# Performance work log

Measured on AMD Instinct MI355X. Metric: run time of the kernel, lower is better.

Reference implementation:

```python
import jax, jax.numpy as jnp
import numpy as np

N, E = 32768, 1048576          # nodes, edges (avg degree 32)
IN, H, OUT = 128, 128, 40       # in_channels, hidden_channels, out_channels
L, R = 3, 16                    # num_layers, n_rules
EPS = 1e-5                      # BatchNorm eps


def setup_inputs() -> dict:
    key = jax.random.key(0)
    ks = jax.random.split(key, 10)
    s_in = 1.0 / np.sqrt(IN)
    s_h = 1.0 / np.sqrt(H)
    return {
        "x": jax.random.normal(ks[0], (N, IN), jnp.float32),
        "edge_index": jax.random.randint(ks[1], (2, E), 0, N, jnp.int32),
        "W_in": jax.random.normal(ks[2], (IN, H), jnp.float32) * s_in,
        "b_in": jnp.zeros((H,), jnp.float32),
        "centers": jax.random.normal(ks[3], (L, R, H), jnp.float32),
        "widths": jax.random.uniform(ks[4], (L, R, H), jnp.float32, 0.5, 1.5),
        "Wc": jax.random.normal(ks[5], (L, R, H, H), jnp.float32) * s_h,
        "bc": jnp.zeros((L, R, H), jnp.float32),
        "bn_gamma": jnp.ones((L, H), jnp.float32),
        "bn_beta": jnp.zeros((L, H), jnp.float32),
        "W_head": jax.random.normal(ks[6], (H, OUT), jnp.float32) * s_h,
        "b_head": jnp.zeros((OUT,), jnp.float32),
    }


def reference(x, edge_index, W_in, b_in, centers, widths, Wc, bc,
              bn_gamma, bn_beta, W_head, b_head):
    src, dst = edge_index[0], edge_index[1]
    n = x.shape[0]
    # in-degree for mean aggregation (clamped to 1)
    deg = jax.ops.segment_sum(jnp.ones(src.shape, x.dtype), dst, num_segments=n)
    deg = jnp.maximum(deg, 1.0)[:, None]

    h = jax.nn.relu(x @ W_in + b_in)  # [N, H]
    for l in range(L):
        # Gaussian rule memberships -> normalized firing strengths [N, R]
        d2 = (h[:, None, :] - centers[l]) ** 2 / (2.0 * widths[l] ** 2)  # [N,R,H]
        w = jax.nn.softmax(-jnp.mean(d2, axis=-1), axis=-1)              # [N,R]
        # TSK rule consequents (per-rule linear) and firing-weighted mix
        y = jnp.einsum('nh,rho->nro', h, Wc[l]) + bc[l]                  # [N,R,H]
        msg = jnp.einsum('nr,nro->no', w, y)                             # [N,H]
        # edge gather (src) + scatter-mean to dst
        agg = jax.ops.segment_sum(msg[src], dst, num_segments=n) / deg   # [N,H]
        # relu -> BatchNorm1d (batch statistics) -> residual (dropout=eval)
        a = jax.nn.relu(agg)
        mu = jnp.mean(a, axis=0)
        var = jnp.var(a, axis=0)
        a = (a - mu) * jax.lax.rsqrt(var + EPS) * bn_gamma[l] + bn_beta[l]
        h = h + a
    return jax.nn.softmax(h @ W_head + b_head, axis=-1)  # [N, OUT]
```

## Files before the change

kernel.cpp:

```cpp
#include <hip/hip_runtime.h>
#include <hip/hip_bf16.h>
#include <stdint.h>


#define NN 32768
#define NE 1048576
#define H 128
#define R 16
#define NL 3
#define ODIM 40
#define NBIN 64
#define BINCAP 18432

typedef short bf16x8 __attribute__((ext_vector_type(8)));
typedef float f32x4 __attribute__((ext_vector_type(4)));
typedef unsigned short u16x4 __attribute__((ext_vector_type(4)));

__device__ inline short f2bf_rne(float f) {
    unsigned u = __float_as_uint(f);
    u += 0x7FFFu + ((u >> 16) & 1u);
    return (short)(u >> 16);
}
__device__ inline void split_bf(float v, short& hi, short& lo) {
    unsigned u = __float_as_uint(v);
    unsigned uh = (u + 0x7FFFu + ((u >> 16) & 1u)) & 0xFFFF0000u;
    hi = (short)(uh >> 16);
    lo = f2bf_rne(v - __uint_as_float(uh));
}
__device__ inline f32x4 bf4f(u16x4 v) {
    f32x4 r;
    r.x = __uint_as_float((unsigned)v.x << 16);
    r.y = __uint_as_float((unsigned)v.y << 16);
    r.z = __uint_as_float((unsigned)v.z << 16);
    r.w = __uint_as_float((unsigned)v.w << 16);
    return r;
}
__device__ inline void gload_lds16(const void* g, void* l) {
    __builtin_amdgcn_global_load_lds(
        (const __attribute__((address_space(1))) unsigned*)g,
        (__attribute__((address_space(3))) unsigned*)l, 16, 0, 0);
}

__device__ inline f32x4 bn4(f32x4 hv, f32x4 av, f32x4 s1, f32x4 s2, f32x4 gm,
                            f32x4 bt) {
    f32x4 r;
#define BN_C(X)                                               \
    {                                                         \
        float mu = s1.X * (1.0f / NN);                        \
        float var = s2.X * (1.0f / NN) - mu * mu;             \
        float inv = rsqrtf(var + 1e-5f);                      \
        r.X = hv.X + (av.X - mu) * inv * gm.X + bt.X;         \
    }
    BN_C(x) BN_C(y) BN_C(z) BN_C(w)
#undef BN_C
    return r;
}

__global__ __launch_bounds__(256) void k_prep_all(
    const float* __restrict__ Wc, short* __restrict__ WcT,
    const float* __restrict__ W_in, short* __restrict__ WinHi,
    short* __restrict__ WinLo, const float* __restrict__ W_head,
    short* __restrict__ WhHi, short* __restrict__ WhLo,
    const float* __restrict__ widths, float* __restrict__ IW,
    int* __restrict__ binCnt) {
    int bid = blockIdx.x, tid = threadIdx.x;
    if (bid < 3072) {
        int s = bid * 256 + tid;
        int lr = s >> 14;
        int rem = s & 16383;
        int k = rem >> 7, o = rem & 127;
        int kb = k >> 3;
        int d = lr * 16384 + o * 128 + (((kb ^ (o & 7)) << 3)) + (k & 7);
        WcT[d] = f2bf_rne(Wc[s]);
    } else if (bid < 3136) {
        int t = (bid - 3072) * 256 + tid;
        int k = t >> 7, o = t & 127;
        int kb = k >> 3;
        int d = o * 128 + (((kb ^ (o & 7)) << 3)) + (k & 7);
        short hi, lo;
        split_bf(W_in[k * 128 + o], hi, lo);
        WinHi[d] = hi;
        WinLo[d] = lo;
    } else if (bid < 3160) {
        int t = (bid - 3136) * 256 + tid;
        int o = t >> 7, k = t & 127;
        float v = (o < ODIM) ? W_head[k * ODIM + o] : 0.0f;
        int kb = k >> 3;
        int d = o * 128 + (((kb ^ (o & 7)) << 3)) + (k & 7);
        short hi, lo;
        split_bf(v, hi, lo);
        WhHi[d] = hi;
        WhLo[d] = lo;
    } else if (bid < 3184) {
        int t = (bid - 3160) * 256 + tid;
        float wd = widths[t];
        IW[t] = 0.5f / (wd * wd) * (1.0f / 128.0f);
    } else {
        if (tid < NBIN) binCnt[tid] = 0;
    }
}

__global__ __launch_bounds__(256) void k_part(const int* __restrict__ src,
                                              const int* __restrict__ dst,
                                              int* __restrict__ binCnt,
                                              int* __restrict__ pbuf) {
    __shared__ int hist[NBIN];
    int tid = threadIdx.x;
    int e0 = blockIdx.x * 8192;
    if (tid < NBIN) hist[tid] = 0;
    __syncthreads();
    for (int i = tid; i < 8192; i += 256)
        atomicAdd(&hist[dst[e0 + i] >> 9], 1);
    __syncthreads();
    if (tid < NBIN) hist[tid] = atomicAdd(&binCnt[tid], hist[tid]);
    __syncthreads();
    for (int i = tid; i < 8192; i += 256) {
        int d = dst[e0 + i], s = src[e0 + i];
        int b = d >> 9;
        int p = atomicAdd(&hist[b], 1);
        pbuf[b * BINCAP + p] = s | ((d & 511) << 15);
    }
}

__global__ __launch_bounds__(64) void k_scan64(const int* __restrict__ binCnt,
                                               int* __restrict__ binStart,
                                               int* __restrict__ row_start,
                                               float* __restrict__ sumsAll) {
    int t = threadIdx.x;
    for (int i = t; i < 768; i += 64) sumsAll[i] = 0.0f;
    int c = binCnt[t];
    int v = c;
    for (int off = 1; off < 64; off <<= 1) {
        int u = __shfl_up(v, off);
        if (t >= off) v += u;
    }
    binStart[t] = v - c;
    if (t == 63) {
        binStart[NBIN] = v;
        row_start[NN] = v;
    }
}

__global__ __launch_bounds__(512) void k_sortp(const int* __restrict__ binCnt,
                                               const int* __restrict__ binStart,
                                               const int* __restrict__ pbuf,
                                               int* __restrict__ esrc,
                                               int* __restrict__ row_start) {
    __shared__ int cnt[512], sc[512], cur[512];
    int b = blockIdx.x, t = threadIdx.x;
    int n = binCnt[b];
    int gbase = binStart[b];
    const int* p = pbuf + b * BINCAP;
    cnt[t] = 0;
    __syncthreads();
    for (int i = t; i < n; i += 512)
        atomicAdd(&cnt[(p[i] >> 15) & 511], 1);
    __syncthreads();
    sc[t] = cnt[t];
    __syncthreads();
    for (int off = 1; off < 512; off <<= 1) {
        int v = (t >= off) ? sc[t - off] : 0;
        __syncthreads();
        sc[t] += v;
        __syncthreads();
    }
    int start = gbase + sc[t] - cnt[t];
    row_start[b * 512 + t] = start;
    cur[t] = start;
    __syncthreads();
    for (int i = t; i < n; i += 512) {
        int e = p[i];
        int pos = atomicAdd(&cur[(e >> 15) & 511], 1);
        esrc[pos] = e & 32767;
    }
}

__global__ __launch_bounds__(256, 2) void k_in_mfma(
    const float* __restrict__ x, const short* __restrict__ Whi,
    const short* __restrict__ Wlo, const float* __restrict__ b,
    float* __restrict__ h) {
    __shared__ short Bs[16384];
    int tid = threadIdx.x, lane = tid & 63, wv = tid >> 6;
    int quad = lane >> 4, lm = lane & 15;
    int row0 = blockIdx.x * 64;
    int m = row0 + wv * 16 + lm;

    bf16x8 ahi[4], alo[4];
#pragma unroll
    for (int kc = 0; kc < 4; kc++) {
        f32x4 va = *(const f32x4*)(x + m * H + kc * 32 + quad * 8);
        f32x4 vb = *(const f32x4*)(x + m * H + kc * 32 + quad * 8 + 4);
        float vv[8] = {va.x, va.y, va.z, va.w, vb.x, vb.y, vb.z, vb.w};
#pragma unroll
        for (int j = 0; j < 8; j++) {
            short hi, lo;
            split_bf(vv[j], hi, lo);
            ahi[kc][j] = hi;
            alo[kc][j] = lo;
        }
    }
    f32x4 acc[8];
#pragma unroll
    for (int c = 0; c < 8; c++) acc[c] = (f32x4){0.f, 0.f, 0.f, 0.f};

    char* ldst = (char*)Bs + wv * 8192;
    const char* g1 = (const char*)Whi + wv * 8192 + lane * 16;
#pragma unroll
    for (int cc = 0; cc < 8; cc++) gload_lds16(g1 + cc * 1024, ldst + cc * 1024);
    __syncthreads();
#pragma unroll
    for (int kc = 0; kc < 4; kc++)
#pragma unroll
        for (int c = 0; c < 8; c++) {
            int o = c * 16 + lm;
            bf16x8 bfr = *(const bf16x8*)&Bs[o * 128 + (((kc * 4 + quad) ^ (o & 7)) << 3)];
            acc[c] = __builtin_amdgcn_mfma_f32_16x16x32_bf16(ahi[kc], bfr, acc[c], 0, 0, 0);
            acc[c] = __builtin_amdgcn_mfma_f32_16x16x32_bf16(alo[kc], bfr, acc[c], 0, 0, 0);
        }
    __syncthreads();
    const char* g2 = (const char*)Wlo + wv * 8192 + lane * 16;
#pragma unroll
    for (int cc = 0; cc < 8; cc++) gload_lds16(g2 + cc * 1024, ldst + cc * 1024);
    __syncthreads();
#pragma unroll
    for (int kc = 0; kc < 4; kc++)
#pragma unroll
        for (int c = 0; c < 8; c++) {
            int o = c * 16 + lm;
            bf16x8 bfr = *(const bf16x8*)&Bs[o * 128 + (((kc * 4 + quad) ^ (o & 7)) << 3)];
            acc[c] = __builtin_amdgcn_mfma_f32_16x16x32_bf16(ahi[kc], bfr, acc[c], 0, 0, 0);
        }
    int orow = row0 + wv * 16 + quad * 4;
#pragma unroll
    for (int c = 0; c < 8; c++) {
        int col = c * 16 + lm;
        float bi = b[col];
#pragma unroll
        for (int v = 0; v < 4; v++)
            h[(orow + v) * H + col] = fmaxf(acc[c][v] + bi, 0.0f);
    }
}

__global__ __launch_bounds__(256, 2) void k_gemm3(
    const float* __restrict__ h, const float* __restrict__ aprev,
    const float* __restrict__ sums, const float* __restrict__ gamma,
    const float* __restrict__ beta, const short* __restrict__ BT,
    const float* __restrict__ bc, const float* __restrict__ cen,
    const float* __restrict__ iw, unsigned short* __restrict__ msgb,
    float* __restrict__ hout) {
    __shared__ __align__(16) char smemu[33792];
    short* Bs = (short*)smemu;
    float(*hs)[132] = (float(*)[132])smemu;
    __shared__ float wsh[16][64];
    __shared__ float sm[64][17];

    int tid = threadIdx.x, lane = tid & 63, wv = tid >> 6;
    int quad = lane >> 4, lm = lane & 15;
    int row0 = blockIdx.x * 64;

    if (gamma) {
        for (int g = tid; g < 2048; g += 256) {
            int rr = g >> 5, cc = (g & 31) << 2;
            int grow = row0 + rr;
            f32x4 hv = *(const f32x4*)&h[grow * H + cc];
            f32x4 av = *(const f32x4*)&aprev[grow * H + cc];
            f32x4 r = bn4(hv, av, *(const f32x4*)&sums[cc],
                          *(const f32x4*)&sums[H + cc],
                          *(const f32x4*)&gamma[cc], *(const f32x4*)&beta[cc]);
            *(f32x4*)&hs[rr][cc] = r;
            *(f32x4*)&hout[grow * H + cc] = r;
        }
    } else {
        const f32x4* hg = (const f32x4*)(h + row0 * H);
        for (int g = tid; g < 2048; g += 256) {
            int rr = g >> 5, cc = (g & 31) << 2;
            *(f32x4*)&hs[rr][cc] = hg[g];
        }
    }
    __syncthreads();

    {
        int wvu = __builtin_amdgcn_readfirstlane(wv);
        const float* c0 = cen + (wvu * 4 + 0) * H;
        const float* c1 = cen + (wvu * 4 + 1) * H;
        const float* c2 = cen + (wvu * 4 + 2) * H;
        const float* c3 = cen + (wvu * 4 + 3) * H;
        const float* w0 = iw + (wvu * 4 + 0) * H;
        const float* w1 = iw + (wvu * 4 + 1) * H;
        const float* w2 = iw + (wvu * 4 + 2) * H;
        const float* w3 = iw + (wvu * 4 + 3) * H;
        float s0 = 0.f, s1 = 0.f, s2 = 0.f, s3 = 0.f;
#pragma unroll 4
        for (int j0 = 0; j0 < H; j0 += 4) {
            f32x4 hv = *(const f32x4*)&hs[lane][j0];
            f32x4 cv, wv4, d;
            cv = *(const f32x4*)(c0 + j0); wv4 = *(const f32x4*)(w0 + j0);
            d = hv - cv;
            s0 += d.x * d.x * wv4.x + d.y * d.y * wv4.y + d.z * d.z * wv4.z + d.w * d.w * wv4.w;
            cv = *(const f32x4*)(c1 + j0); wv4 = *(const f32x4*)(w1 + j0);
            d = hv - cv;
            s1 += d.x * d.x * wv4.x + d.y * d.y * wv4.y + d.z * d.z * wv4.z + d.w * d.w * wv4.w;
            cv = *(const f32x4*)(c2 + j0); wv4 = *(const f32x4*)(w2 + j0);
            d = hv - cv;
            s2 += d.x * d.x * wv4.x + d.y * d.y * wv4.y + d.z * d.z * wv4.z + d.w * d.w * wv4.w;
            cv = *(const f32x4*)(c3 + j0); wv4 = *(const f32x4*)(w3 + j0);
            d = hv - cv;
            s3 += d.x * d.x * wv4.x + d.y * d.y * wv4.y + d.z * d.z * wv4.z + d.w * d.w * wv4.w;
        }
        sm[lane][wvu * 4 + 0] = s0;
        sm[lane][wvu * 4 + 1] = s1;
        sm[lane][wvu * 4 + 2] = s2;
        sm[lane][wvu * 4 + 3] = s3;
    }

    bf16x8 ahi[4], alo[4];
    {
        int m = wv * 16 + lm;
#pragma unroll
        for (int kc = 0; kc < 4; kc++) {
            f32x4 va = *(const f32x4*)&hs[m][kc * 32 + quad * 8];
            f32x4 vb = *(const f32x4*)&hs[m][kc * 32 + quad * 8 + 4];
            float vv[8] = {va.x, va.y, va.z, va.w, vb.x, vb.y, vb.z, vb.w};
#pragma unroll
            for (int j = 0; j < 8; j++) {
                short hi, lo;
                split_bf(vv[j], hi, lo);
                ahi[kc][j] = hi;
                alo[kc][j] = lo;
            }
        }
    }
    __syncthreads();

    if (tid < 64) {
        float v[16], mx = -1e30f;
#pragma unroll
        for (int r = 0; r < R; r++) {
            v[r] = -sm[tid][r];
            mx = fmaxf(mx, v[r]);
        }
        float sum = 0.f, e[16];
#pragma unroll
        for (int r = 0; r < R; r++) {
            e[r] = __expf(v[r] - mx);
            sum += e[r];
        }
        float inv = 1.0f / sum;
#pragma unroll
        for (int r = 0; r < R; r++) wsh[r][tid] = e[r] * inv;
    }

    f32x4 out[8];
#pragma unroll
    for (int c = 0; c < 8; c++) out[c] = (f32x4){0.f, 0.f, 0.f, 0.f};

    char* ldst = (char*)Bs + wv * 8192;
    for (int r = 0; r < R; r++) {
        __syncthreads();
        const char* gsrc = (const char*)(BT + r * 16384) + wv * 8192 + lane * 16;
#pragma unroll
        for (int cc = 0; cc < 8; cc++) gload_lds16(gsrc + cc * 1024, ldst + cc * 1024);
        __syncthreads();

        f32x4 accr[8];
#pragma unroll
        for (int c = 0; c < 8; c++) accr[c] = (f32x4){0.f, 0.f, 0.f, 0.f};
#pragma unroll
        for (int kc = 0; kc < 4; kc++)
#pragma unroll
            for (int c = 0; c < 8; c++) {
                int o = c * 16 + lm;
                bf16x8 bfr = *(const bf16x8*)&Bs[o * 128 + (((kc * 4 + quad) ^ (o & 7)) << 3)];
                accr[c] = __builtin_amdgcn_mfma_f32_16x16x32_bf16(ahi[kc], bfr, accr[c], 0, 0, 0);
                accr[c] = __builtin_amdgcn_mfma_f32_16x16x32_bf16(alo[kc], bfr, accr[c], 0, 0, 0);
            }
        f32x4 wr4 = *(const f32x4*)&wsh[r][wv * 16 + quad * 4];
#pragma unroll
        for (int c = 0; c < 8; c++) {
            out[c].x += wr4.x * accr[c].x;
            out[c].y += wr4.y * accr[c].y;
            out[c].z += wr4.z * accr[c].z;
            out[c].w += wr4.w * accr[c].w;
        }
    }

    __syncthreads();
    for (int g = tid; g < 512; g += 256) {
        int o = g >> 2, kb = g & 3;
        bf16x8 v;
#pragma unroll
        for (int j = 0; j < 8; j++) {
            int k = kb * 8 + j;
            v[j] = (k < R) ? f2bf_rne(bc[k * H + o]) : (short)0;
        }
        *(bf16x8*)&Bs[o * 128 + ((kb ^ (o & 7)) << 3)] = v;
    }
    bf16x8 abias;
#pragma unroll
    for (int j = 0; j < 8; j++)
        abias[j] = (quad < 2) ? f2bf_rne(wsh[quad * 8 + j][wv * 16 + lm]) : (short)0;
    __syncthreads();
#pragma unroll
    for (int c = 0; c < 8; c++) {
        int o = c * 16 + lm;
        bf16x8 bfr = *(const bf16x8*)&Bs[o * 128 + ((quad ^ (o & 7)) << 3)];
        out[c] = __builtin_amdgcn_mfma_f32_16x16x32_bf16(abias, bfr, out[c], 0, 0, 0);
    }

    int orow = row0 + wv * 16 + quad * 4;
#pragma unroll
    for (int c = 0; c < 8; c++) {
        int col = c * 16 + lm;
#pragma unroll
        for (int v = 0; v < 4; v++)
            msgb[(orow + v) * H + col] = (unsigned short)f2bf_rne(out[c][v]);
    }
}

__global__ __launch_bounds__(256) void k_agg(
    const unsigned short* __restrict__ msgb, const int* __restrict__ row_start,
    const int* __restrict__ esrc, float* __restrict__ a) {
    int tid = threadIdx.x;
    int g = tid >> 5, lane = tid & 31;
    int n = blockIdx.x * 8 + g;
    int b = row_start[n], e = row_start[n + 1];
    f32x4 a0 = {0.f, 0.f, 0.f, 0.f}, a1 = a0, a2 = a0, a3 = a0;
    f32x4 a4 = a0, a5 = a0, a6 = a0, a7 = a0;
    int i = b;
    for (; i + 8 <= e; i += 8) {
        int s0 = esrc[i], s1 = esrc[i + 1], s2 = esrc[i + 2], s3 = esrc[i + 3];
        int s4 = esrc[i + 4], s5 = esrc[i + 5], s6 = esrc[i + 6], s7 = esrc[i + 7];
        a0 += bf4f(*(const u16x4*)&msgb[s0 * H + lane * 4]);
        a1 += bf4f(*(const u16x4*)&msgb[s1 * H + lane * 4]);
        a2 += bf4f(*(const u16x4*)&msgb[s2 * H + lane * 4]);
        a3 += bf4f(*(const u16x4*)&msgb[s3 * H + lane * 4]);
        a4 += bf4f(*(const u16x4*)&msgb[s4 * H + lane * 4]);
        a5 += bf4f(*(const u16x4*)&msgb[s5 * H + lane * 4]);
        a6 += bf4f(*(const u16x4*)&msgb[s6 * H + lane * 4]);
        a7 += bf4f(*(const u16x4*)&msgb[s7 * H + lane * 4]);
    }
    for (; i < e; i++)
        a0 += bf4f(*(const u16x4*)&msgb[esrc[i] * H + lane * 4]);
    f32x4 t = ((a0 + a1) + (a2 + a3)) + ((a4 + a5) + (a6 + a7));
    float id = 1.0f / fmaxf((float)(e - b), 1.0f);
    f32x4 res;
    res.x = fmaxf(t.x * id, 0.f);
    res.y = fmaxf(t.y * id, 0.f);
    res.z = fmaxf(t.z * id, 0.f);
    res.w = fmaxf(t.w * id, 0.f);
    *(f32x4*)&a[n * H + lane * 4] = res;
}

__global__ __launch_bounds__(128) void k_bnstats(const float* __restrict__ a,
                                                 float* __restrict__ sums) {
    int t = threadIdx.x;
    float s = 0.0f, s2 = 0.0f;
    for (int n = blockIdx.x; n < NN; n += gridDim.x) {
        float v = a[n * H + t];
        s += v;
        s2 += v * v;
    }
    atomicAdd(&sums[t], s);
    atomicAdd(&sums[H + t], s2);
}

__global__ __launch_bounds__(256, 2) void k_head2(
    const float* __restrict__ h, const float* __restrict__ aprev,
    const float* __restrict__ sums, const float* __restrict__ gamma,
    const float* __restrict__ beta, const short* __restrict__ Whi,
    const short* __restrict__ Wlo, const float* __restrict__ bh,
    float* __restrict__ out) {
    __shared__ short Bs[12288];
    int tid = threadIdx.x, lane = tid & 63, wv = tid >> 6;
    int quad = lane >> 4, lm = lane & 15;
    int row0 = blockIdx.x * 64;
    int m = row0 + wv * 16 + lm;

    bf16x8 ahi[4], alo[4];
#pragma unroll
    for (int kc = 0; kc < 4; kc++) {
        int base = kc * 32 + quad * 8;
        f32x4 hv0 = *(const f32x4*)&h[m * H + base];
        f32x4 hv1 = *(const f32x4*)&h[m * H + base + 4];
        f32x4 av0 = *(const f32x4*)&aprev[m * H + base];
        f32x4 av1 = *(const f32x4*)&aprev[m * H + base + 4];
        f32x4 r0 = bn4(hv0, av0, *(const f32x4*)&sums[base],
                       *(const f32x4*)&sums[H + base],
                       *(const f32x4*)&gamma[base], *(const f32x4*)&beta[base]);
        f32x4 r1 = bn4(hv1, av1, *(const f32x4*)&sums[base + 4],
                       *(const f32x4*)&sums[H + base + 4],
                       *(const f32x4*)&gamma[base + 4],
                       *(const f32x4*)&beta[base + 4]);
        float vv[8] = {r0.x, r0.y, r0.z, r0.w, r1.x, r1.y, r1.z, r1.w};
#pragma unroll
        for (int j = 0; j < 8; j++) {
            short hi, lo;
            split_bf(vv[j], hi, lo);
            ahi[kc][j] = hi;
            alo[kc][j] = lo;
        }
    }
    {
        char* ldst = (char*)Bs + wv * 3072;
        const char* g1 = (const char*)Whi + wv * 3072 + lane * 16;
        const char* g2 = (const char*)Wlo + wv * 3072 + lane * 16;
#pragma unroll
        for (int cc = 0; cc < 3; cc++) gload_lds16(g1 + cc * 1024, ldst + cc * 1024);
        char* ldst2 = (char*)Bs + 12288 + wv * 3072;
#pragma unroll
        for (int cc = 0; cc < 3; cc++) gload_lds16(g2 + cc * 1024, ldst2 + cc * 1024);
    }
    __syncthreads();
    f32x4 acc[3];
#pragma unroll
    for (int c = 0; c < 3; c++) acc[c] = (f32x4){0.f, 0.f, 0.f, 0.f};
#pragma unroll
    for (int kc = 0; kc < 4; kc++)
#pragma unroll
        for (int c = 0; c < 3; c++) {
            int o = c * 16 + lm;
            int off = o * 128 + (((kc * 4 + quad) ^ (o & 7)) << 3);
            bf16x8 bH = *(const bf16x8*)&Bs[off];
            bf16x8 bL = *(const bf16x8*)&Bs[6144 + off];
            acc[c] = __builtin_amdgcn_mfma_f32_16x16x32_bf16(ahi[kc], bH, acc[c], 0, 0, 0);
            acc[c] = __builtin_amdgcn_mfma_f32_16x16x32_bf16(alo[kc], bH, acc[c], 0, 0, 0);
            acc[c] = __builtin_amdgcn_mfma_f32_16x16x32_bf16(ahi[kc], bL, acc[c], 0, 0, 0);
        }
    float bh0 = bh[lm], bh1 = bh[16 + lm];
    float bh2 = (lm < 8) ? bh[32 + lm] : 0.f;
    int orow = row0 + wv * 16 + quad * 4;
#pragma unroll
    for (int v = 0; v < 4; v++) {
        float v0 = acc[0][v] + bh0;
        float v1 = acc[1][v] + bh1;
        float v2 = (lm < 8) ? (acc[2][v] + bh2) : -1e30f;
        float mx = fmaxf(fmaxf(v0, v1), v2);
        for (int off = 8; off; off >>= 1) mx = fmaxf(mx, __shfl_xor(mx, off, 16));
        float e0 = __expf(v0 - mx), e1 = __expf(v1 - mx);
        float e2 = (lm < 8) ? __expf(v2 - mx) : 0.f;
        float s = e0 + e1 + e2;
        for (int off = 8; off; off >>= 1) s += __shfl_xor(s, off, 16);
        float inv = 1.0f / s;
        out[(orow + v) * ODIM + lm] = e0 * inv;
        out[(orow + v) * ODIM + 16 + lm] = e1 * inv;
        if (lm < 8) out[(orow + v) * ODIM + 32 + lm] = e2 * inv;
    }
}

extern "C" void kernel_launch(void* const* d_in, const int* in_sizes, int n_in,
                              void* d_out, int out_size, void* d_ws, size_t ws_size,
                              hipStream_t stream) {
    const float* x = (const float*)d_in[0];
    const int* edge_index = (const int*)d_in[1];
    const float* W_in = (const float*)d_in[2];
    const float* b_in = (const float*)d_in[3];
    const float* centers = (const float*)d_in[4];
    const float* widths = (const float*)d_in[5];
    const float* Wc = (const float*)d_in[6];
    const float* bc = (const float*)d_in[7];
    const float* bn_gamma = (const float*)d_in[8];
    const float* bn_beta = (const float*)d_in[9];
    const float* W_head = (const float*)d_in[10];
    const float* b_head = (const float*)d_in[11];
    float* out = (float*)d_out;

    const int* src = edge_index;
    const int* dst = edge_index + NE;

    float* h = (float*)d_ws;
    float* a = h + NN * H;
    float* sumsAll = a + NN * H;
    float* IW = sumsAll + 768;
    int* binCnt = (int*)(IW + NL * R * H);
    int* binStart = binCnt + NBIN;
    int* row_start = binStart + NBIN + 1;
    int* pbuf = row_start + NN + 1;
    int* esrc = pbuf + NBIN * BINCAP;
    uintptr_t p = (uintptr_t)(esrc + NE);
    p = (p + 63) & ~(uintptr_t)63;
    unsigned short* msgb = (unsigned short*)p;
    short* WcT = (short*)(msgb + NN * H);
    short* WinHi = WcT + NL * R * H * H;
    short* WinLo = WinHi + 16384;
    short* WhHi = WinLo + 16384;
    short* WhLo = WhHi + 6144;

    k_prep_all<<<3185, 256, 0, stream>>>(Wc, WcT, W_in, WinHi, WinLo, W_head,
                                         WhHi, WhLo, widths, IW, binCnt);
    k_part<<<NE / 8192, 256, 0, stream>>>(src, dst, binCnt, pbuf);
    k_scan64<<<1, 64, 0, stream>>>(binCnt, binStart, row_start, sumsAll);
    k_sortp<<<NBIN, 512, 0, stream>>>(binCnt, binStart, pbuf, esrc, row_start);

    k_in_mfma<<<NN / 64, 256, 0, stream>>>(x, WinHi, WinLo, b_in, h);

    for (int l = 0; l < NL; l++) {
        const float* gm = (l == 0) ? nullptr : bn_gamma + (l - 1) * H;
        const float* bt = (l == 0) ? nullptr : bn_beta + (l - 1) * H;
        const float* sm = (l == 0) ? nullptr : sumsAll + 256 * (l - 1);
        k_gemm3<<<NN / 64, 256, 0, stream>>>(h, a, sm, gm, bt,
                                             WcT + l * R * H * H, bc + l * R * H,
                                             centers + l * R * H, IW + l * R * H,
                                             msgb, h);
        k_agg<<<NN / 8, 256, 0, stream>>>(msgb, row_start, esrc, a);
        k_bnstats<<<512, 128, 0, stream>>>(a, sumsAll + 256 * l);
    }
    k_head2<<<NN / 64, 256, 0, stream>>>(h, a, sumsAll + 512, bn_gamma + 2 * H,
                                         bn_beta + 2 * H, WhHi, WhLo, b_head, out);
}
```

Baseline: 509.8 us.

## Double-buffer rule weight loads in k_gemm3 and fuse BN stats into aggregation

Result: slower. 1.525 ms (+199.2%).

```diff
diff --git a/kernel.cpp b/kernel.cpp
--- a/kernel.cpp
+++ b/kernel.cpp
@@ -248,9 +248,8 @@
     const float* __restrict__ bc, const float* __restrict__ cen,
     const float* __restrict__ iw, unsigned short* __restrict__ msgb,
     float* __restrict__ hout) {
-    __shared__ __align__(16) char smemu[33792];
-    short* Bs = (short*)smemu;
-    float(*hs)[132] = (float(*)[132])smemu;
+    __shared__ __align__(16) char smem[65536];
+    float(*hs)[132] = (float(*)[132])smem;
     __shared__ float wsh[16][64];
     __shared__ float sm[64][17];
 
@@ -350,17 +349,27 @@
         for (int r = 0; r < R; r++) wsh[r][tid] = e[r] * inv;
     }
 
+    {
+        const char* gsrc = (const char*)BT + wv * 8192 + lane * 16;
+        char* ld = smem + wv * 8192;
+#pragma unroll
+        for (int cc = 0; cc < 8; cc++) gload_lds16(gsrc + cc * 1024, ld + cc * 1024);
+    }
+    __syncthreads();
+
     f32x4 out[8];
 #pragma unroll
     for (int c = 0; c < 8; c++) out[c] = (f32x4){0.f, 0.f, 0.f, 0.f};
 
-    char* ldst = (char*)Bs + wv * 8192;
     for (int r = 0; r < R; r++) {
-        __syncthreads();
-        const char* gsrc = (const char*)(BT + r * 16384) + wv * 8192 + lane * 16;
-#pragma unroll
-        for (int cc = 0; cc < 8; cc++) gload_lds16(gsrc + cc * 1024, ldst + cc * 1024);
-        __syncthreads();
+        if (r + 1 < R) {
+            const char* gsrc = (const char*)(BT + (r + 1) * 16384) + wv * 8192 + lane * 16;
+            char* ld = smem + ((r + 1) & 1) * 32768 + wv * 8192;
+#pragma unroll
+            for (int cc = 0; cc < 8; cc++)
+                gload_lds16(gsrc + cc * 1024, ld + cc * 1024);
+        }
+        const short* Bcur = (const short*)(smem + (r & 1) * 32768);
 
         f32x4 accr[8];
 #pragma unroll
@@ -370,7 +379,7 @@
 #pragma unroll
             for (int c = 0; c < 8; c++) {
                 int o = c * 16 + lm;
-                bf16x8 bfr = *(const bf16x8*)&Bs[o * 128 + (((kc * 4 + quad) ^ (o & 7)) << 3)];
+                bf16x8 bfr = *(const bf16x8*)&Bcur[o * 128 + (((kc * 4 + quad) ^ (o & 7)) << 3)];
                 accr[c] = __builtin_amdgcn_mfma_f32_16x16x32_bf16(ahi[kc], bfr, accr[c], 0, 0, 0);
                 accr[c] = __builtin_amdgcn_mfma_f32_16x16x32_bf16(alo[kc], bfr, accr[c], 0, 0, 0);
             }
@@ -382,9 +391,10 @@
             out[c].z += wr4.z * accr[c].z;
             out[c].w += wr4.w * accr[c].w;
         }
-    }
-
-    __syncthreads();
+        __syncthreads();
+    }
+
+    short* Bs0 = (short*)smem;
     for (int g = tid; g < 512; g += 256) {
         int o = g >> 2, kb = g & 3;
         bf16x8 v;
@@ -393,7 +403,7 @@
             int k = kb * 8 + j;
             v[j] = (k < R) ? f2bf_rne(bc[k * H + o]) : (short)0;
         }
-        *(bf16x8*)&Bs[o * 128 + ((kb ^ (o & 7)) << 3)] = v;
+        *(bf16x8*)&Bs0[o * 128 + ((kb ^ (o & 7)) << 3)] = v;
     }
     bf16x8 abias;
 #pragma unroll
@@ -403,7 +413,7 @@
 #pragma unroll
     for (int c = 0; c < 8; c++) {
         int o = c * 16 + lm;
-        bf16x8 bfr = *(const bf16x8*)&Bs[o * 128 + ((quad ^ (o & 7)) << 3)];
+        bf16x8 bfr = *(const bf16x8*)&Bs0[o * 128 + ((quad ^ (o & 7)) << 3)];
         out[c] = __builtin_amdgcn_mfma_f32_16x16x32_bf16(abias, bfr, out[c], 0, 0, 0);
     }
 
@@ -419,7 +429,10 @@
 
 __global__ __launch_bounds__(256) void k_agg(
     const unsigned short* __restrict__ msgb, const int* __restrict__ row_start,
-    const int* __restrict__ esrc, float* __restrict__ a) {
+    const int* __restrict__ esrc, float* __restrict__ a,
+    float* __restrict__ sums) {
+    __shared__ f32x4 red1[8][32];
+    __shared__ f32x4 red2[8][32];
     int tid = threadIdx.x;
     int g = tid >> 5, lane = tid & 31;
     int n = blockIdx.x * 8 + g;
@@ -449,19 +462,28 @@
     res.z = fmaxf(t.z * id, 0.f);
     res.w = fmaxf(t.w * id, 0.f);
     *(f32x4*)&a[n * H + lane * 4] = res;
-}
-
-__global__ __launch_bounds__(128) void k_bnstats(const float* __restrict__ a,
-                                                 float* __restrict__ sums) {
-    int t = threadIdx.x;
-    float s = 0.0f, s2 = 0.0f;
-    for (int n = blockIdx.x; n < NN; n += gridDim.x) {
-        float v = a[n * H + t];
-        s += v;
-        s2 += v * v;
-    }
-    atomicAdd(&sums[t], s);
-    atomicAdd(&sums[H + t], s2);
+    red1[g][lane] = res;
+    f32x4 r2 = {res.x * res.x, res.y * res.y, res.z * res.z, res.w * res.w};
+    red2[g][lane] = r2;
+    __syncthreads();
+    int c0 = lane * 4;
+    if (g == 0) {
+        f32x4 t1 = red1[0][lane];
+#pragma unroll
+        for (int gg = 1; gg < 8; gg++) t1 += red1[gg][lane];
+        atomicAdd(&sums[c0], t1.x);
+        atomicAdd(&sums[c0 + 1], t1.y);
+        atomicAdd(&sums[c0 + 2], t1.z);
+        atomicAdd(&sums[c0 + 3], t1.w);
+    } else if (g == 1) {
+        f32x4 t2 = red2[0][lane];
+#pragma unroll
+        for (int gg = 1; gg < 8; gg++) t2 += red2[gg][lane];
+        atomicAdd(&sums[H + c0], t2.x);
+        atomicAdd(&sums[H + c0 + 1], t2.y);
+        atomicAdd(&sums[H + c0 + 2], t2.z);
+        atomicAdd(&sums[H + c0 + 3], t2.w);
+    }
 }
 
 __global__ __launch_bounds__(256, 2) void k_head2(
@@ -601,8 +623,8 @@
                                              WcT + l * R * H * H, bc + l * R * H,
                                              centers + l * R * H, IW + l * R * H,
                                              msgb, h);
-        k_agg<<<NN / 8, 256, 0, stream>>>(msgb, row_start, esrc, a);
-        k_bnstats<<<512, 128, 0, stream>>>(a, sumsAll + 256 * l);
+        k_agg<<<NN / 8, 256, 0, stream>>>(msgb, row_start, esrc, a,
+                                          sumsAll + 256 * l);
     }
     k_head2<<<NN / 64, 256, 0, stream>>>(h, a, sumsAll + 512, bn_gamma + 2 * H,
                                          bn_beta + 2 * H, WhHi, WhLo, b_head, out);
```
